# Optimization experiments

Measured on AMD Instinct MI355X. Metric: run time of the kernel, lower is better.

## Reference

```python
import jax, jax.numpy as jnp
import numpy as np

N_NODES = 100000
HEADS = 4
NEG_SLOPE = 0.2


def setup_inputs() -> dict:
    key = jax.random.key(0)
    ks = jax.random.split(key, 16)
    in_dim, hidden, emb = 128, 64, 64
    hc = hidden // HEADS  # per-head channels layer1
    ec = emb // HEADS     # per-head channels layer2

    def glorot(k, shape):
        fan = shape[0] + shape[-1]
        lim = jnp.sqrt(6.0 / fan)
        return jax.random.uniform(k, shape, jnp.float32, -lim, lim)

    x = jax.random.normal(ks[0], (N_NODES, in_dim), jnp.float32)
    edge_index = jax.random.randint(ks[1], (2, 1600000), 0, N_NODES, jnp.int64)
    return {
        "x": x,
        "edge_index": edge_index,
        "W1": glorot(ks[2], (in_dim, hidden)),
        "a1_src": glorot(ks[3], (HEADS, hc)),
        "a1_dst": glorot(ks[4], (HEADS, hc)),
        "b1": jnp.zeros((hidden,), jnp.float32),
        "W2": glorot(ks[5], (hidden, emb)),
        "a2_src": glorot(ks[6], (HEADS, ec)),
        "a2_dst": glorot(ks[7], (HEADS, ec)),
        "b2": jnp.zeros((emb,), jnp.float32),
        "Wp": glorot(ks[8], (emb, emb)),
        "bp": jnp.zeros((emb,), jnp.float32),
    }


def gat_layer(x, src, dst, W, a_src, a_dst, b):
    """PyG GATConv (concat=True, add_self_loops already in src/dst, no dropout/eval)."""
    N = x.shape[0]
    H, C = a_src.shape
    xw = (x @ W).reshape(N, H, C)                       # [N,H,C]
    al_src = jnp.einsum('nhc,hc->nh', xw, a_src)        # [N,H]
    al_dst = jnp.einsum('nhc,hc->nh', xw, a_dst)
    e = al_src[src] + al_dst[dst]                       # [E,H]
    e = jnp.where(e > 0, e, NEG_SLOPE * e)              # leaky_relu
    # segment softmax over incoming edges of each destination node
    m = jax.ops.segment_max(e, dst, num_segments=N)     # [N,H]
    m = jnp.where(jnp.isfinite(m), m, 0.0)
    ee = jnp.exp(e - m[dst])
    s = jax.ops.segment_sum(ee, dst, num_segments=N)    # [N,H]
    alpha = ee / (s[dst] + 1e-16)                       # [E,H]
    msg = xw[src] * alpha[:, :, None]                   # [E,H,C]
    out = jax.ops.segment_sum(msg, dst, num_segments=N) # [N,H,C]
    return out.reshape(N, H * C) + b


def reference(x, edge_index, W1, a1_src, a1_dst, b1, W2, a2_src, a2_dst, b2, Wp, bp):
    N = x.shape[0]
    loops = jnp.arange(N, dtype=edge_index.dtype)
    src = jnp.concatenate([edge_index[0], loops])
    dst = jnp.concatenate([edge_index[1], loops])
    h = jax.nn.elu(gat_layer(x, src, dst, W1, a1_src, a1_dst, b1))
    h = gat_layer(h, src, dst, W2, a2_src, a2_dst, b2)
    return jax.nn.elu(h) @ Wp + bp
```

## Files before the change

kernel.cpp:

```cpp
#include <hip/hip_runtime.h>
#include <hip/hip_bf16.h>
#include <math.h>

#define NEG_SLOPE 0.2f
#define BCAP 6144
#define ECHUNK 8192

typedef __bf16 bf16x8 __attribute__((ext_vector_type(8)));
typedef float  f32x4  __attribute__((ext_vector_type(4)));

__device__ __forceinline__ unsigned short f2b(float f) {
    union { float f; unsigned u; } c; c.f = f;
    unsigned r = (c.u + 0x7fffu + ((c.u >> 16) & 1u)) >> 16;
    return (unsigned short)r;
}
__device__ __forceinline__ float b2f(unsigned short s) {
    union { unsigned u; float f; } c; c.u = ((unsigned)s) << 16;
    return c.f;
}

__global__ __launch_bounds__(256) void k_feat1(
    const float* __restrict__ x, const float* __restrict__ W1,
    const float* __restrict__ a_src, const float* __restrict__ a_dst,
    unsigned short* __restrict__ xwb, float* __restrict__ als, float* __restrict__ ald,
    int* __restrict__ bcur, int NB, int N)
{
    int t = threadIdx.x;
    int gid = blockIdx.x * 256 + t;
    if (gid < NB) bcur[gid] = 0;

    __shared__ unsigned short WT[64][136];
    for (int f = t; f < 128 * 64; f += 256) {
        int k = f >> 6, c = f & 63;
        WT[c][k] = f2b(W1[f]);
    }
    __syncthreads();
    int wave = t >> 6, lane = t & 63;
    int lrow = lane & 15, lgrp = lane >> 4;
    int r0 = blockIdx.x * 64 + wave * 16;
    if (r0 >= N) return;

    bf16x8 bf[4][4];
#pragma unroll
    for (int ct = 0; ct < 4; ++ct)
#pragma unroll
        for (int ks = 0; ks < 4; ++ks)
            bf[ct][ks] = *(const bf16x8*)&WT[ct * 16 + lrow][ks * 32 + lgrp * 8];

    f32x4 acc[4];
#pragma unroll
    for (int ct = 0; ct < 4; ++ct) acc[ct] = (f32x4){0.f, 0.f, 0.f, 0.f};

    int rowA = r0 + lrow; if (rowA >= N) rowA = N - 1;
    const float* xp = x + (size_t)rowA * 128 + lgrp * 8;
#pragma unroll
    for (int ks = 0; ks < 4; ++ks) {
        f32x4 v0 = *(const f32x4*)(xp + ks * 32);
        f32x4 v1 = *(const f32x4*)(xp + ks * 32 + 4);
        union { unsigned short s[8]; bf16x8 b; } af;
        af.s[0] = f2b(v0[0]); af.s[1] = f2b(v0[1]); af.s[2] = f2b(v0[2]); af.s[3] = f2b(v0[3]);
        af.s[4] = f2b(v1[0]); af.s[5] = f2b(v1[1]); af.s[6] = f2b(v1[2]); af.s[7] = f2b(v1[3]);
#pragma unroll
        for (int ct = 0; ct < 4; ++ct)
            acc[ct] = __builtin_amdgcn_mfma_f32_16x16x32_bf16(af.b, bf[ct][ks], acc[ct], 0, 0, 0);
    }

    float asv[4], adv[4];
#pragma unroll
    for (int ct = 0; ct < 4; ++ct) { asv[ct] = a_src[ct * 16 + lrow]; adv[ct] = a_dst[ct * 16 + lrow]; }
#pragma unroll
    for (int q = 0; q < 4; ++q) {
        int row = r0 + lgrp * 4 + q;
        bool ok = row < N;
#pragma unroll
        for (int ct = 0; ct < 4; ++ct) {
            float v = acc[ct][q];
            if (ok) xwb[(size_t)row * 64 + ct * 16 + lrow] = f2b(v);
            float ps = v * asv[ct], pd = v * adv[ct];
#pragma unroll
            for (int m = 1; m < 16; m <<= 1) {
                ps += __shfl_xor(ps, m, 64);
                pd += __shfl_xor(pd, m, 64);
            }
            if (ok && lrow == 0) { als[row * 4 + ct] = ps; ald[row * 4 + ct] = pd; }
        }
    }
}

__global__ __launch_bounds__(256) void k_feat2(
    const unsigned short* __restrict__ hb, const float* __restrict__ W,
    const float* __restrict__ a_src, const float* __restrict__ a_dst,
    unsigned short* __restrict__ xwb, float* __restrict__ als, float* __restrict__ ald, int N)
{
    __shared__ unsigned short WT[64][72];
    int t = threadIdx.x;
    for (int f = t; f < 64 * 64; f += 256) {
        int k = f >> 6, c = f & 63;
        WT[c][k] = f2b(W[f]);
    }
    __syncthreads();
    int wave = t >> 6, lane = t & 63;
    int lrow = lane & 15, lgrp = lane >> 4;
    int r0 = blockIdx.x * 64 + wave * 16;
    if (r0 >= N) return;

    bf16x8 bf[4][2];
#pragma unroll
    for (int ct = 0; ct < 4; ++ct)
#pragma unroll
        for (int ks = 0; ks < 2; ++ks)
            bf[ct][ks] = *(const bf16x8*)&WT[ct * 16 + lrow][ks * 32 + lgrp * 8];

    f32x4 acc[4];
#pragma unroll
    for (int ct = 0; ct < 4; ++ct) acc[ct] = (f32x4){0.f, 0.f, 0.f, 0.f};

    int rowA = r0 + lrow; if (rowA >= N) rowA = N - 1;
    const unsigned short* hp = hb + (size_t)rowA * 64 + lgrp * 8;
#pragma unroll
    for (int ks = 0; ks < 2; ++ks) {
        bf16x8 af = *(const bf16x8*)(hp + ks * 32);
#pragma unroll
        for (int ct = 0; ct < 4; ++ct)
            acc[ct] = __builtin_amdgcn_mfma_f32_16x16x32_bf16(af, bf[ct][ks], acc[ct], 0, 0, 0);
    }

    float asv[4], adv[4];
#pragma unroll
    for (int ct = 0; ct < 4; ++ct) { asv[ct] = a_src[ct * 16 + lrow]; adv[ct] = a_dst[ct * 16 + lrow]; }
#pragma unroll
    for (int q = 0; q < 4; ++q) {
        int row = r0 + lgrp * 4 + q;
        bool ok = row < N;
#pragma unroll
        for (int ct = 0; ct < 4; ++ct) {
            float v = acc[ct][q];
            if (ok) xwb[(size_t)row * 64 + ct * 16 + lrow] = f2b(v);
            float ps = v * asv[ct], pd = v * adv[ct];
#pragma unroll
            for (int m = 1; m < 16; m <<= 1) {
                ps += __shfl_xor(ps, m, 64);
                pd += __shfl_xor(pd, m, 64);
            }
            if (ok && lrow == 0) { als[row * 4 + ct] = ps; ald[row * 4 + ct] = pd; }
        }
    }
}

__global__ __launch_bounds__(256) void k_proj(
    const unsigned short* __restrict__ gb, const float* __restrict__ Wp,
    const float* __restrict__ bp, float* __restrict__ out, int N)
{
    __shared__ unsigned short WT[64][72];
    int t = threadIdx.x;
    for (int f = t; f < 64 * 64; f += 256) {
        int k = f >> 6, c = f & 63;
        WT[c][k] = f2b(Wp[f]);
    }
    __syncthreads();
    int wave = t >> 6, lane = t & 63;
    int lrow = lane & 15, lgrp = lane >> 4;
    int r0 = blockIdx.x * 64 + wave * 16;
    if (r0 >= N) return;

    bf16x8 bf[4][2];
#pragma unroll
    for (int ct = 0; ct < 4; ++ct)
#pragma unroll
        for (int ks = 0; ks < 2; ++ks)
            bf[ct][ks] = *(const bf16x8*)&WT[ct * 16 + lrow][ks * 32 + lgrp * 8];

    f32x4 acc[4];
#pragma unroll
    for (int ct = 0; ct < 4; ++ct) acc[ct] = (f32x4){0.f, 0.f, 0.f, 0.f};

    int rowA = r0 + lrow; if (rowA >= N) rowA = N - 1;
    const unsigned short* gp = gb + (size_t)rowA * 64 + lgrp * 8;
#pragma unroll
    for (int ks = 0; ks < 2; ++ks) {
        bf16x8 af = *(const bf16x8*)(gp + ks * 32);
#pragma unroll
        for (int ct = 0; ct < 4; ++ct)
            acc[ct] = __builtin_amdgcn_mfma_f32_16x16x32_bf16(af, bf[ct][ks], acc[ct], 0, 0, 0);
    }

    float bpv[4];
#pragma unroll
    for (int ct = 0; ct < 4; ++ct) bpv[ct] = bp[ct * 16 + lrow];
#pragma unroll
    for (int q = 0; q < 4; ++q) {
        int row = r0 + lgrp * 4 + q;
        if (row >= N) break;
#pragma unroll
        for (int ct = 0; ct < 4; ++ct)
            out[(size_t)row * 64 + ct * 16 + lrow] = acc[ct][q] + bpv[ct];
    }
}

__global__ __launch_bounds__(256) void k_bucket(const int* __restrict__ src, const int* __restrict__ dst,
                                                int* __restrict__ bcur, unsigned* __restrict__ bbuf,
                                                int E, int NB) {
    __shared__ int cnt[512];
    __shared__ int base[512];
    int t = threadIdx.x;
    int e0 = blockIdx.x * ECHUNK;
    int e1 = e0 + ECHUNK; if (e1 > E) e1 = E;
    for (int i = t; i < NB; i += 256) cnt[i] = 0;
    __syncthreads();
    for (int i = e0 + t; i < e1; i += 256) atomicAdd(&cnt[dst[i] >> 8], 1);
    __syncthreads();
    for (int i = t; i < NB; i += 256) {
        int c = cnt[i];
        base[i] = c ? atomicAdd(&bcur[i], c) : 0;
        cnt[i] = 0;
    }
    __syncthreads();
    for (int i = e0 + t; i < e1; i += 256) {
        int d = dst[i];
        int b = d >> 8;
        int rel = atomicAdd(&cnt[b], 1);
        int pos = base[b] + rel;
        if (pos < BCAP)
            bbuf[(size_t)b * BCAP + pos] = ((unsigned)src[i] << 8) | (unsigned)(d & 255);
    }
}

__global__ __launch_bounds__(256) void k_bdeg(const int* __restrict__ bcur, const unsigned* __restrict__ bbuf,
                                              int* __restrict__ deg, int N) {
    __shared__ int cnt[256];
    int t = threadIdx.x, b = blockIdx.x;
    cnt[t] = 1;
    __syncthreads();
    int nb = bcur[b]; if (nb > BCAP) nb = BCAP;
    const unsigned* bp = bbuf + (size_t)b * BCAP;
    for (int j = t; j < nb; j += 256) atomicAdd(&cnt[bp[j] & 255u], 1);
    __syncthreads();
    int node = b * 256 + t;
    if (node < N) deg[node] = cnt[t];
}

__global__ __launch_bounds__(256) void k_blocksum(const int* __restrict__ deg, int* __restrict__ partial, int N) {
    __shared__ int red[256];
    int t = threadIdx.x;
    int idx = blockIdx.x * 256 + t;
    red[t] = (idx < N) ? deg[idx] : 0;
    __syncthreads();
    for (int off = 128; off > 0; off >>= 1) {
        if (t < off) red[t] += red[t + off];
        __syncthreads();
    }
    if (t == 0) partial[blockIdx.x] = red[0];
}

__global__ __launch_bounds__(512) void k_scanpartials(int* __restrict__ partial, int nb) {
    __shared__ int ts[512];
    int t = threadIdx.x;
    int v = (t < nb) ? partial[t] : 0;
    ts[t] = v;
    __syncthreads();
    for (int off = 1; off < 512; off <<= 1) {
        int u = (t >= off) ? ts[t - off] : 0;
        __syncthreads();
        ts[t] += u;
        __syncthreads();
    }
    if (t < nb) partial[t] = ts[t] - v;
}

__global__ __launch_bounds__(256) void k_writeoffs(const int* __restrict__ deg, const int* __restrict__ partial,
                                                   int* __restrict__ offs, int N) {
    __shared__ int ts[256];
    int t = threadIdx.x;
    int idx = blockIdx.x * 256 + t;
    int d = (idx < N) ? deg[idx] : 0;
    ts[t] = d;
    __syncthreads();
    for (int off = 1; off < 256; off <<= 1) {
        int u = (t >= off) ? ts[t - off] : 0;
        __syncthreads();
        ts[t] += u;
        __syncthreads();
    }
    int off_ = partial[blockIdx.x] + ts[t] - d;
    if (idx < N) {
        offs[idx] = off_;
        if (idx == N - 1) offs[N] = off_ + d;
    }
}

__global__ __launch_bounds__(256) void k_place(const int* __restrict__ bcur, const unsigned* __restrict__ bbuf,
                                               const int* __restrict__ offs, int* __restrict__ ssrc, int N) {
    __shared__ int curld[256];
    __shared__ int offld[256];
    int t = threadIdx.x, b = blockIdx.x;
    int node = b * 256 + t;
    int o = (node < N) ? offs[node] : 0;
    offld[t] = o;
    curld[t] = 1;
    if (node < N) ssrc[o] = node;
    __syncthreads();
    int nb = bcur[b]; if (nb > BCAP) nb = BCAP;
    const unsigned* bp = bbuf + (size_t)b * BCAP;
    for (int j = t; j < nb; j += 256) {
        unsigned v = bp[j];
        int dl = v & 255u;
        int rel = atomicAdd(&curld[dl], 1);
        ssrc[offld[dl] + rel] = (int)(v >> 8);
    }
}

__global__ __launch_bounds__(256) void k_aggregate(
    const int* __restrict__ offs, const int* __restrict__ ssrc,
    const unsigned short* __restrict__ xwb, const float* __restrict__ alsrc,
    const float* __restrict__ aldst, const float* __restrict__ bias,
    unsigned short* __restrict__ hout, int N)
{
    __shared__ float wls[4][32 * 8];
    int t = threadIdx.x;
    int wave = t >> 6, lane = t & 63;
    int n = blockIdx.x * 4 + wave;
    if (n >= N) return;
    int half = lane >> 5;
    int cl = lane & 31;
    int hp = cl >> 3;
    int s0 = offs[n], s1 = offs[n + 1];
    f32x4 adv = *(const f32x4*)(aldst + (size_t)n * 4);
    float* wl = wls[wave];
    int* wli = (int*)wl;
    const char* xb = (const char*)xwb;
    float ssum = 0.f, acc0 = 0.f, acc1 = 0.f;

    for (int c0 = s0; c0 < s1; c0 += 32) {
        int nb = s1 - c0; if (nb > 32) nb = 32;
        if (lane < nb) {
            int s = ssrc[c0 + lane];
            f32x4 al = *(const f32x4*)(alsrc + (size_t)s * 4);
            int o8 = lane * 8;
            int ob = s << 7;
#pragma unroll
            for (int q = 0; q < 4; ++q) {
                float e = al[q] + adv[q];
                e = fmaxf(e, NEG_SLOPE * e);
                wl[o8 + 2 * q] = __expf(fminf(e, 60.f));
                wli[o8 + 2 * q + 1] = ob;
            }
        }
        int e = 0;
        for (; e + 8 <= nb; e += 8) {
#pragma unroll
            for (int u = 0; u < 4; ++u) {
                int idx = e + 2 * u + half;
                int bo = idx * 8 + hp * 2;
                float w = wl[bo];
                int   o = wli[bo + 1];
                unsigned pv = *(const unsigned*)(xb + o + cl * 4);
                union { unsigned u_; float f; } lo, hi;
                lo.u_ = pv << 16;
                hi.u_ = pv & 0xffff0000u;
                ssum += w;
                acc0 = fmaf(w, lo.f, acc0);
                acc1 = fmaf(w, hi.f, acc1);
            }
        }
        for (; e < nb; e += 2) {
            int idx = e + half;
            if (idx < nb) {
                int bo = idx * 8 + hp * 2;
                float w = wl[bo];
                int   o = wli[bo + 1];
                unsigned pv = *(const unsigned*)(xb + o + cl * 4);
                union { unsigned u_; float f; } lo, hi;
                lo.u_ = pv << 16;
                hi.u_ = pv & 0xffff0000u;
                ssum += w;
                acc0 = fmaf(w, lo.f, acc0);
                acc1 = fmaf(w, hi.f, acc1);
            }
        }
    }

    ssum += __shfl_xor(ssum, 32, 64);
    acc0 += __shfl_xor(acc0, 32, 64);
    acc1 += __shfl_xor(acc1, 32, 64);
    float inv = 1.f / ssum;
    float2 bv = *(const float2*)(bias + 2 * cl);
    float h0 = fmaf(acc0, inv, bv.x);
    float h1 = fmaf(acc1, inv, bv.y);
    h0 = h0 > 0.f ? h0 : expm1f(h0);
    h1 = h1 > 0.f ? h1 : expm1f(h1);
    if (!half) {
        union { unsigned short s2[2]; unsigned u; } st;
        st.s2[0] = f2b(h0); st.s2[1] = f2b(h1);
        *(unsigned*)((char*)hout + ((size_t)n * 64 + cl * 2) * 2) = st.u;
    }
}

extern "C" void kernel_launch(void* const* d_in, const int* in_sizes, int n_in,
                              void* d_out, int out_size, void* d_ws, size_t ws_size,
                              hipStream_t stream) {
    const float* x   = (const float*)d_in[0];
    const int*   ei  = (const int*)d_in[1];
    const float* W1  = (const float*)d_in[2];
    const float* a1s = (const float*)d_in[3];
    const float* a1d = (const float*)d_in[4];
    const float* b1  = (const float*)d_in[5];
    const float* W2  = (const float*)d_in[6];
    const float* a2s = (const float*)d_in[7];
    const float* a2d = (const float*)d_in[8];
    const float* b2  = (const float*)d_in[9];
    const float* Wp  = (const float*)d_in[10];
    const float* bp  = (const float*)d_in[11];
    float* out = (float*)d_out;

    const int N = in_sizes[0] / 128;
    const int E = in_sizes[1] / 2;
    const int Etot = E + N;
    const int NB = (N + 255) >> 8;
    const int* esrc = ei;
    const int* edst = ei + E;

    char* p = (char*)d_ws;
    auto alloc = [&](size_t bytes) {
        char* r = p;
        p += (bytes + 255) & ~(size_t)255;
        return (void*)r;
    };
    unsigned short* xw1b = (unsigned short*)alloc((size_t)N * 64 * 2);
    unsigned short* xw2b = (unsigned short*)alloc((size_t)N * 64 * 2);
    unsigned short* h1b  = (unsigned short*)alloc((size_t)N * 64 * 2);
    unsigned short* h2b  = (unsigned short*)alloc((size_t)N * 64 * 2);
    float* al1sv = (float*)alloc((size_t)N * 4 * 4);
    float* al1dv = (float*)alloc((size_t)N * 4 * 4);
    float* al2sv = (float*)alloc((size_t)N * 4 * 4);
    float* al2dv = (float*)alloc((size_t)N * 4 * 4);
    int*   deg   = (int*)alloc((size_t)N * 4);
    int*   offs  = (int*)alloc((size_t)(N + 1) * 4);
    int*   ssrc  = (int*)alloc((size_t)Etot * 4);
    int*   part  = (int*)alloc((size_t)512 * 4);
    int*   bcur  = (int*)alloc((size_t)NB * 4);
    unsigned* bbuf = (unsigned*)alloc((size_t)NB * BCAP * 4);
    (void)ws_size; (void)n_in; (void)out_size;

    dim3 blk(256);
    int gN256 = (N + 255) / 256;
    int gEchunk = (E + ECHUNK - 1) / ECHUNK;
    int gN4   = (N + 3) / 4;
    int gN64  = (N + 63) / 64;

    k_feat1<<<gN64, blk, 0, stream>>>(x, W1, a1s, a1d, xw1b, al1sv, al1dv, bcur, NB, N);
    k_bucket<<<gEchunk, blk, 0, stream>>>(esrc, edst, bcur, bbuf, E, NB);
    k_bdeg<<<NB, blk, 0, stream>>>(bcur, bbuf, deg, N);
    k_blocksum<<<gN256, blk, 0, stream>>>(deg, part, N);
    k_scanpartials<<<1, 512, 0, stream>>>(part, gN256);
    k_writeoffs<<<gN256, blk, 0, stream>>>(deg, part, offs, N);
    k_place<<<NB, blk, 0, stream>>>(bcur, bbuf, offs, ssrc, N);
    k_aggregate<<<gN4, blk, 0, stream>>>(offs, ssrc, xw1b, al1sv, al1dv, b1, h1b, N);
    k_feat2<<<gN64, blk, 0, stream>>>(h1b, W2, a2s, a2d, xw2b, al2sv, al2dv, N);
    k_aggregate<<<gN4, blk, 0, stream>>>(offs, ssrc, xw2b, al2sv, al2dv, b2, h2b, N);
    k_proj<<<gN64, blk, 0, stream>>>(h2b, Wp, bp, out, N);
}
```

Before: 215.6 us.

## Fuse CSR construction into bucket-base scan plus single per-bucket kernel

Replaces the five-kernel CSR build (per-node degree, block sums, partial scan, offset write, placement) with two kernels. A single-block scan computes each bucket's base from bucket counts plus self-loops. A per-bucket kernel then stages the bucket's edges in LDS, counts degrees, scans locally, writes offsets and places sources. This removes three launches and a second global read of the bucket buffer, at the cost of about 24KB of LDS per block, which may reduce occupancy.

Result: faster. 208.8 us (-3.2%).

```diff
diff --git a/kernel.cpp b/kernel.cpp
--- a/kernel.cpp
+++ b/kernel.cpp
@@ -225,37 +225,16 @@
     }
 }
 
-__global__ __launch_bounds__(256) void k_bdeg(const int* __restrict__ bcur, const unsigned* __restrict__ bbuf,
-                                              int* __restrict__ deg, int N) {
-    __shared__ int cnt[256];
-    int t = threadIdx.x, b = blockIdx.x;
-    cnt[t] = 1;
-    __syncthreads();
-    int nb = bcur[b]; if (nb > BCAP) nb = BCAP;
-    const unsigned* bp = bbuf + (size_t)b * BCAP;
-    for (int j = t; j < nb; j += 256) atomicAdd(&cnt[bp[j] & 255u], 1);
-    __syncthreads();
-    int node = b * 256 + t;
-    if (node < N) deg[node] = cnt[t];
-}
-
-__global__ __launch_bounds__(256) void k_blocksum(const int* __restrict__ deg, int* __restrict__ partial, int N) {
-    __shared__ int red[256];
-    int t = threadIdx.x;
-    int idx = blockIdx.x * 256 + t;
-    red[t] = (idx < N) ? deg[idx] : 0;
-    __syncthreads();
-    for (int off = 128; off > 0; off >>= 1) {
-        if (t < off) red[t] += red[t + off];
-        __syncthreads();
-    }
-    if (t == 0) partial[blockIdx.x] = red[0];
-}
-
-__global__ __launch_bounds__(512) void k_scanpartials(int* __restrict__ partial, int nb) {
+__global__ __launch_bounds__(512) void k_scanbases(const int* __restrict__ bcur, int* __restrict__ bbase,
+                                                   int NB, int N) {
     __shared__ int ts[512];
     int t = threadIdx.x;
-    int v = (t < nb) ? partial[t] : 0;
+    int v = 0;
+    if (t < NB) {
+        int nb = bcur[t]; if (nb > BCAP) nb = BCAP;
+        int vn = N - t * 256; if (vn > 256) vn = 256; if (vn < 0) vn = 0;
+        v = nb + vn;
+    }
     ts[t] = v;
     __syncthreads();
     for (int off = 1; off < 512; off <<= 1) {
@@ -264,48 +243,50 @@
         ts[t] += u;
         __syncthreads();
     }
-    if (t < nb) partial[t] = ts[t] - v;
-}
-
-__global__ __launch_bounds__(256) void k_writeoffs(const int* __restrict__ deg, const int* __restrict__ partial,
-                                                   int* __restrict__ offs, int N) {
-    __shared__ int ts[256];
-    int t = threadIdx.x;
-    int idx = blockIdx.x * 256 + t;
-    int d = (idx < N) ? deg[idx] : 0;
-    ts[t] = d;
-    __syncthreads();
-    for (int off = 1; off < 256; off <<= 1) {
-        int u = (t >= off) ? ts[t - off] : 0;
-        __syncthreads();
-        ts[t] += u;
-        __syncthreads();
-    }
-    int off_ = partial[blockIdx.x] + ts[t] - d;
-    if (idx < N) {
-        offs[idx] = off_;
-        if (idx == N - 1) offs[N] = off_ + d;
-    }
-}
-
-__global__ __launch_bounds__(256) void k_place(const int* __restrict__ bcur, const unsigned* __restrict__ bbuf,
-                                               const int* __restrict__ offs, int* __restrict__ ssrc, int N) {
-    __shared__ int curld[256];
-    __shared__ int offld[256];
+    if (t < NB) bbase[t] = ts[t] - v;
+}
+
+__global__ __launch_bounds__(256) void k_csr(const int* __restrict__ bcur, const unsigned* __restrict__ bbuf,
+                                             const int* __restrict__ bbase,
+                                             int* __restrict__ offs, int* __restrict__ ssrc, int N) {
+    __shared__ unsigned ebuf[BCAP];
+    __shared__ int cnt[256];
+    __shared__ int scn[256];
     int t = threadIdx.x, b = blockIdx.x;
     int node = b * 256 + t;
-    int o = (node < N) ? offs[node] : 0;
-    offld[t] = o;
-    curld[t] = 1;
-    if (node < N) ssrc[o] = node;
-    __syncthreads();
     int nb = bcur[b]; if (nb > BCAP) nb = BCAP;
     const unsigned* bp = bbuf + (size_t)b * BCAP;
+    cnt[t] = (node < N) ? 1 : 0;
+    __syncthreads();
     for (int j = t; j < nb; j += 256) {
         unsigned v = bp[j];
+        ebuf[j] = v;
+        atomicAdd(&cnt[v & 255u], 1);
+    }
+    __syncthreads();
+    int d = cnt[t];
+    scn[t] = d;
+    __syncthreads();
+    for (int off = 1; off < 256; off <<= 1) {
+        int u = (t >= off) ? scn[t - off] : 0;
+        __syncthreads();
+        scn[t] += u;
+        __syncthreads();
+    }
+    int o = bbase[b] + scn[t] - d;
+    if (node < N) {
+        offs[node] = o;
+        ssrc[o] = node;
+        if (node == N - 1) offs[N] = o + d;
+    }
+    __syncthreads();
+    cnt[t] = o + 1;
+    __syncthreads();
+    for (int j = t; j < nb; j += 256) {
+        unsigned v = ebuf[j];
         int dl = v & 255u;
-        int rel = atomicAdd(&curld[dl], 1);
-        ssrc[offld[dl] + rel] = (int)(v >> 8);
+        int pos = atomicAdd(&cnt[dl], 1);
+        ssrc[pos] = (int)(v >> 8);
     }
 }
 
@@ -433,27 +414,22 @@
     float* al1dv = (float*)alloc((size_t)N * 4 * 4);
     float* al2sv = (float*)alloc((size_t)N * 4 * 4);
     float* al2dv = (float*)alloc((size_t)N * 4 * 4);
-    int*   deg   = (int*)alloc((size_t)N * 4);
     int*   offs  = (int*)alloc((size_t)(N + 1) * 4);
     int*   ssrc  = (int*)alloc((size_t)Etot * 4);
-    int*   part  = (int*)alloc((size_t)512 * 4);
     int*   bcur  = (int*)alloc((size_t)NB * 4);
+    int*   bbase = (int*)alloc((size_t)(NB + 1) * 4);
     unsigned* bbuf = (unsigned*)alloc((size_t)NB * BCAP * 4);
     (void)ws_size; (void)n_in; (void)out_size;
 
     dim3 blk(256);
-    int gN256 = (N + 255) / 256;
     int gEchunk = (E + ECHUNK - 1) / ECHUNK;
     int gN4   = (N + 3) / 4;
     int gN64  = (N + 63) / 64;
 
     k_feat1<<<gN64, blk, 0, stream>>>(x, W1, a1s, a1d, xw1b, al1sv, al1dv, bcur, NB, N);
     k_bucket<<<gEchunk, blk, 0, stream>>>(esrc, edst, bcur, bbuf, E, NB);
-    k_bdeg<<<NB, blk, 0, stream>>>(bcur, bbuf, deg, N);
-    k_blocksum<<<gN256, blk, 0, stream>>>(deg, part, N);
-    k_scanpartials<<<1, 512, 0, stream>>>(part, gN256);
-    k_writeoffs<<<gN256, blk, 0, stream>>>(deg, part, offs, N);
-    k_place<<<NB, blk, 0, stream>>>(bcur, bbuf, offs, ssrc, N);
+    k_scanbases<<<1, 512, 0, stream>>>(bcur, bbase, NB, N);
+    k_csr<<<NB, blk, 0, stream>>>(bcur, bbuf, bbase, offs, ssrc, N);
     k_aggregate<<<gN4, blk, 0, stream>>>(offs, ssrc, xw1b, al1sv, al1dv, b1, h1b, N);
     k_feat2<<<gN64, blk, 0, stream>>>(h1b, W2, a2s, a2d, xw2b, al2sv, al2dv, N);
     k_aggregate<<<gN4, blk, 0, stream>>>(offs, ssrc, xw2b, al2sv, al2dv, b2, h2b, N);
```
